# Optimization experiments

Hardware: AMD Instinct MI355X
Metric: run time of the kernel (lower is better)

The kernel has to match this reference:

```python
import jax, jax.numpy as jnp
import numpy as np

B, N, NPOINT, NSAMPLE = 4, 8192, 2048, 32
RADIUS = 0.5
IN_DIM, OUT_DIM, EXP = 64, 128, 4
GROUPS, EPS = 8, 1e-5


def fps(xyz, npoint):
    # xyz: [B,3,N] -> idx [B,npoint]. Deterministic start at index 0
    # (torch version uses a random start; math otherwise identical).
    b, _, n = xyz.shape
    binds = jnp.arange(b)

    def step(carry, _):
        dist_min, far = carry
        centroid = xyz[binds, :, far]                      # [B,3]
        d = jnp.sum((xyz - centroid[:, :, None]) ** 2, 1)  # [B,N]
        dist_min = jnp.minimum(dist_min, d)
        new_far = jnp.argmax(dist_min, axis=-1).astype(jnp.int32)
        return (dist_min, new_far), far

    init = (jnp.full((b, n), 1e10, dtype=xyz.dtype), jnp.zeros((b,), jnp.int32))
    _, idx = jax.lax.scan(step, init, None, length=npoint)
    return idx.T  # [B, npoint]


def gather(points, idx):
    # points: [B,C,N], idx: [B, ...] -> [B, C, ...]
    return jax.vmap(lambda p, i: p[:, i])(points, idx)


def ball_query(radius, nsample, xyz, new_xyz):
    # xyz: [B,3,N], new_xyz: [B,3,S] -> group_idx [B,S,nsample]
    n = xyz.shape[2]
    sq_s = jnp.sum(new_xyz ** 2, axis=1)  # [B,S]
    sq_n = jnp.sum(xyz ** 2, axis=1)      # [B,N]
    d = sq_s[:, :, None] + sq_n[:, None, :] - 2.0 * jnp.einsum('bcs,bcn->bsn', new_xyz, xyz)
    ar = jnp.arange(n, dtype=jnp.int32)
    idxv = jnp.where(d <= radius * radius, ar[None, None, :], n)  # out-of-ball -> N
    neg, _ = jax.lax.top_k(-idxv, nsample)  # nsample smallest indices
    gi = -neg                               # ascending, matches sort()[..., :nsample]
    first = gi[:, :, :1]
    first = jnp.where(first == n, 0, first)
    gi = jnp.where(gi == n, first, gi)
    return gi


def group_norm(x, gamma, beta):
    # x: [B,C,*spatial]; normalize per (group, all spatial)
    b, c = x.shape[0], x.shape[1]
    sp = x.shape[2:]
    xg = x.reshape(b, GROUPS, -1)
    mu = xg.mean(-1, keepdims=True)
    var = xg.var(-1, keepdims=True)
    xg = (xg - mu) * jax.lax.rsqrt(var + EPS)
    x = xg.reshape(b, c, *sp)
    gshape = (1, c) + (1,) * len(sp)
    return x * gamma.reshape(gshape) + beta.reshape(gshape)


def setup_inputs() -> dict:
    key = jax.random.key(0)
    ks = jax.random.split(key, 10)
    sc = lambda k, shape, s: jax.random.normal(k, shape, jnp.float32) * s
    ed = OUT_DIM * EXP
    return {
        'xyz': jax.random.normal(ks[0], (B, 3, N), jnp.float32),
        'points': jax.random.normal(ks[1], (B, IN_DIM, N), jnp.float32),
        't_emb': jax.random.normal(ks[2], (B, OUT_DIM), jnp.float32),
        'c_emb': jax.random.normal(ks[3], (B, OUT_DIM), jnp.float32),
        'w_mlp': sc(ks[4], (OUT_DIM, IN_DIM + 3), 0.1), 'b_mlp': jnp.zeros((OUT_DIM,), jnp.float32),
        'g0': jnp.ones((OUT_DIM,), jnp.float32), 'be0': jnp.zeros((OUT_DIM,), jnp.float32),
        'w1': sc(ks[5], (ed, OUT_DIM), 0.1), 'b1': jnp.zeros((ed,), jnp.float32),
        'g1': jnp.ones((ed,), jnp.float32), 'be1': jnp.zeros((ed,), jnp.float32),
        'w2': sc(ks[6], (OUT_DIM, ed), 0.1), 'b2': jnp.zeros((OUT_DIM,), jnp.float32),
        'g2': jnp.ones((OUT_DIM,), jnp.float32), 'be2': jnp.zeros((OUT_DIM,), jnp.float32),
        'wt': sc(ks[7], (2 * OUT_DIM, OUT_DIM), 0.02), 'bt': jnp.zeros((2 * OUT_DIM,), jnp.float32),
        'wc': sc(ks[8], (2 * OUT_DIM, OUT_DIM), 0.02), 'bc': jnp.zeros((2 * OUT_DIM,), jnp.float32),
    }


def reference(xyz, points, t_emb, c_emb, w_mlp, b_mlp, g0, be0, w1, b1, g1, be1, w2, b2, g2, be2, wt, bt, wc, bc):
    idx = fps(xyz, NPOINT)              # [B,S]
    new_xyz = gather(xyz, idx)          # [B,3,S]
    gi = ball_query(RADIUS, NSAMPLE, xyz, new_xyz)   # [B,S,ns]
    grouped_xyz = gather(xyz, gi)                    # [B,3,S,ns]
    gxn = grouped_xyz - new_xyz[:, :, :, None]
    gp = gather(points, gi)                          # [B,C,S,ns]
    feat = jnp.concatenate([gxn, gp], axis=1)        # [B,C+3,S,ns]
    x = jnp.einsum('oc,bcsk->bosk', w_mlp, feat) + b_mlp[None, :, None, None]
    x = jax.nn.silu(group_norm(x, g0, be0))
    x = x.max(axis=3)                                # [B,O,S]
    # InvResMLP with dual FiLM
    identity = x
    h = jnp.einsum('oc,bcs->bos', w1, x) + b1[None, :, None]
    h = jax.nn.silu(group_norm(h, g1, be1))
    h = jnp.einsum('oc,bcs->bos', w2, h) + b2[None, :, None]
    h = group_norm(h, g2, be2)
    st, sht = jnp.split(t_emb @ wt.T + bt, 2, axis=1)
    sc_, shc = jnp.split(c_emb @ wc.T + bc, 2, axis=1)
    scale = (st + sc_)[:, :, None]
    shift = (sht + shc)[:, :, None]
    new_points = h * (1.0 + scale) + shift + identity
    return (new_xyz, new_points)
```

## Files before the change

### kernel.cpp

```cpp
#include <hip/hip_runtime.h>
#include <math.h>

#define BB 4
#define NN 8192
#define SS 2048
#define KK 32
#define NGR 8

__global__ void k_sqn(const float* __restrict__ xyz, float* __restrict__ sqn) {
  int i = blockIdx.x * 256 + threadIdx.x;
  if (i >= BB * NN) return;
  int b = i >> 13, n = i & (NN - 1);
  const float* p = xyz + (size_t)b * 3 * NN;
  float x = p[n], y = p[NN + n], z = p[2 * NN + n];
  sqn[i] = __fadd_rn(__fadd_rn(__fmul_rn(x, x), __fmul_rn(y, y)), __fmul_rn(z, z));
}

__global__ void k_tr(const float* __restrict__ pts, float* __restrict__ ptst) {
  __shared__ float tile[64][65];
  int b = blockIdx.y;
  int n0 = blockIdx.x * 64;
  int t = threadIdx.x;
  {
    int n = t & 63, cq = t >> 6;
    for (int j = 0; j < 16; ++j) {
      int c = cq * 16 + j;
      tile[c][n] = pts[((size_t)b * 64 + c) * NN + n0 + n];
    }
  }
  __syncthreads();
  {
    int c = t & 63, nq = t >> 6;
    for (int j = 0; j < 16; ++j) {
      int nn2 = nq * 16 + j;
      ptst[((size_t)b * NN + n0 + nn2) * 64 + c] = tile[c][nn2];
    }
  }
}

__global__ void k_wt(const float* __restrict__ src, float* __restrict__ dst, int rows, int cols) {
  int i = blockIdx.x * 256 + threadIdx.x;
  if (i >= rows * cols) return;
  int r = i / cols, c = i - r * cols;
  dst[c * rows + r] = src[i];
}

__global__ void k_mod(const float* __restrict__ te, const float* __restrict__ ce,
                      const float* __restrict__ wt, const float* __restrict__ bt,
                      const float* __restrict__ wc, const float* __restrict__ bc,
                      float* __restrict__ scl, float* __restrict__ shf) {
  int t = blockIdx.x * 256 + threadIdx.x;
  if (t >= BB * 128) return;
  int b = t >> 7, o = t & 127;
  const float* tb = te + b * 128;
  const float* cb = ce + b * 128;
  float s1 = 0.f, s2 = 0.f, h1 = 0.f, h2 = 0.f;
  for (int c = 0; c < 128; ++c) {
    float tv = tb[c], cv = cb[c];
    s1 = fmaf(tv, wt[o * 128 + c], s1);
    h1 = fmaf(tv, wt[(o + 128) * 128 + c], h1);
    s2 = fmaf(cv, wc[o * 128 + c], s2);
    h2 = fmaf(cv, wc[(o + 128) * 128 + c], h2);
  }
  scl[t] = s1 + bt[o] + s2 + bc[o];
  shf[t] = h1 + bt[o + 128] + h2 + bc[o + 128];
}

template <int CTRL>
__device__ __forceinline__ unsigned long long kmax_dpp(unsigned long long key) {
  int lo = (int)(unsigned)(key & 0xffffffffull);
  int hi = (int)(unsigned)(key >> 32);
  int olo = __builtin_amdgcn_update_dpp(lo, lo, CTRL, 0xf, 0xf, false);
  int ohi = __builtin_amdgcn_update_dpp(hi, hi, CTRL, 0xf, 0xf, false);
  unsigned long long other =
      ((unsigned long long)(unsigned)ohi << 32) | (unsigned)olo;
  return other > key ? other : key;
}

#define FT 512
#define FPT (NN / FT)
#define FW (FT / 64)

__global__ __launch_bounds__(FT, 1) void k_fps(const float* __restrict__ xyz,
                                               float* __restrict__ newxyz) {
  int b = blockIdx.x;
  int t = threadIdx.x;
  const float* gx = xyz + (size_t)b * 3 * NN;
  const float* gy = gx + NN;
  const float* gz = gx + 2 * NN;
  __shared__ float4 p4[NN];
  __shared__ unsigned long long wk[2][FW];
  __shared__ int fars[SS];
  for (int i = t; i < NN; i += FT)
    p4[i] = make_float4(gx[i], gy[i], gz[i], 0.f);
  float px[FPT], py[FPT], pz[FPT], dm[FPT];
#pragma unroll
  for (int j = 0; j < FPT; ++j) {
    px[j] = gx[t + j * FT];
    py[j] = gy[t + j * FT];
    pz[j] = gz[t + j * FT];
    dm[j] = 1e10f;
    asm volatile("" : "+v"(px[j]), "+v"(py[j]), "+v"(pz[j]));
  }
  __syncthreads();
  int far = 0;
  for (int k = 0; k < SS; ++k) {
    float4 c = p4[far];
    if (t == 0) fars[k] = far;
    float bv = -1.f;
    int jb = 0;
#pragma unroll
    for (int j = 0; j < FPT; ++j) {
      float dx = __fsub_rn(px[j], c.x);
      float dy = __fsub_rn(py[j], c.y);
      float dz = __fsub_rn(pz[j], c.z);
      float d = __fadd_rn(__fadd_rn(__fmul_rn(dx, dx), __fmul_rn(dy, dy)), __fmul_rn(dz, dz));
      float m = fminf(dm[j], d);
      dm[j] = m;
      if (m > bv) { bv = m; jb = j; }
    }
    int bp = t + jb * FT;
    unsigned long long key =
        ((unsigned long long)__float_as_uint(bv) << 32) | (unsigned)(NN - 1 - bp);
    key = kmax_dpp<0xB1>(key);
    key = kmax_dpp<0x4E>(key);
    key = kmax_dpp<0x141>(key);
    key = kmax_dpp<0x140>(key);
    key = kmax_dpp<0x142>(key);
    key = kmax_dpp<0x143>(key);
    if ((t & 63) == 63) wk[k & 1][t >> 6] = key;
    __syncthreads();
    unsigned long long kg = wk[k & 1][t & (FW - 1)];
    kg = kmax_dpp<0xB1>(kg);
    kg = kmax_dpp<0x4E>(kg);
    kg = kmax_dpp<0x141>(kg);
    far = NN - 1 - (int)(unsigned)(kg & 0xffffffffull);
    far = __builtin_amdgcn_readfirstlane(far);
  }
  __syncthreads();
  float* ox = newxyz + (size_t)b * 3 * SS;
  for (int k = t; k < SS; k += FT) {
    float4 c = p4[fars[k]];
    ox[k] = c.x; ox[SS + k] = c.y; ox[2 * SS + k] = c.z;
  }
}

__global__ __launch_bounds__(256) void k_ballq(const float* __restrict__ xyz,
                                               const float* __restrict__ sqn,
                                               const float* __restrict__ newxyz,
                                               int* __restrict__ gi) {
  int wid = (blockIdx.x * 256 + threadIdx.x) >> 6;
  int lane = threadIdx.x & 63;
  if (wid >= BB * SS) return;
  int b = wid >> 11, s = wid & (SS - 1);
  const float* nx = newxyz + (size_t)b * 3 * SS;
  float sx = nx[s], sy = nx[SS + s], sz = nx[2 * SS + s];
  float ss = __fadd_rn(__fadd_rn(__fmul_rn(sx, sx), __fmul_rn(sy, sy)), __fmul_rn(sz, sz));
  const float* gx = xyz + (size_t)b * 3 * NN;
  const float* gy = gx + NN;
  const float* gz = gx + 2 * NN;
  const float* sn = sqn + (size_t)b * NN;
  int* go = gi + (size_t)wid * KK;
  int found = 0, first = 0;
  for (int n0 = 0; n0 < NN && found < KK; n0 += 64) {
    int n = n0 + lane;
    float x = gx[n], y = gy[n], z = gz[n];
    float ip = __fmul_rn(sx, x);
    ip = __fmaf_rn(sy, y, ip);
    ip = __fmaf_rn(sz, z, ip);
    float d = __fsub_rn(__fadd_rn(ss, sn[n]), __fmul_rn(2.0f, ip));
    bool pred = (d <= 0.25f);
    unsigned long long m = __ballot(pred);
    if (found == 0 && m) first = n0 + __ffsll((unsigned long long)m) - 1;
    if (pred) {
      int pos = found + __popcll(m & ((1ull << lane) - 1ull));
      if (pos < KK) go[pos] = n;
    }
    found += __popcll(m);
  }
  for (int p = found + lane; p < KK; p += 64) go[p] = first;
}

template <int PASS>
__global__ __launch_bounds__(256) void k_mlp0(
    const float* __restrict__ xyz, const float* __restrict__ ptst,
    const float* __restrict__ newxyz, const int* __restrict__ gi,
    const float* __restrict__ w0, const float* __restrict__ b0,
    double* __restrict__ dst, const float* __restrict__ fmu, const float* __restrict__ frs,
    const float* __restrict__ g0, const float* __restrict__ be0,
    float* __restrict__ xp) {
  __shared__ __align__(16) float w0L[128 * 67];
  __shared__ __align__(16) float featL[67 * 36];
  __shared__ int giL[KK];
  __shared__ float sS[NGR], sQ[NGR];
  __shared__ float maxL[128];
  int t = threadIdx.x;
  int bs = blockIdx.x;
  int b = bs >> 11;
  int s = bs & (SS - 1);
  for (int i = t; i < 128 * 67; i += 256) w0L[i] = w0[i];
  if (t < KK) giL[t] = gi[(size_t)bs * KK + t];
  if (PASS == 0 && t < NGR) { sS[t] = 0.f; sQ[t] = 0.f; }
  __syncthreads();
  {
    int k = t & 31, q = t >> 5;
    int idx = giL[k];
    const float4* src = (const float4*)(ptst + ((size_t)b * NN + idx) * 64 + q * 8);
    float4 v0 = src[0], v1 = src[1];
    int cb = 3 + q * 8;
    featL[(cb + 0) * 36 + k] = v0.x;
    featL[(cb + 1) * 36 + k] = v0.y;
    featL[(cb + 2) * 36 + k] = v0.z;
    featL[(cb + 3) * 36 + k] = v0.w;
    featL[(cb + 4) * 36 + k] = v1.x;
    featL[(cb + 5) * 36 + k] = v1.y;
    featL[(cb + 6) * 36 + k] = v1.z;
    featL[(cb + 7) * 36 + k] = v1.w;
    if (q == 0) {
      const float* gx = xyz + (size_t)b * 3 * NN;
      const float* nx = newxyz + (size_t)b * 3 * SS;
      featL[0 * 36 + k] = gx[idx] - nx[s];
      featL[1 * 36 + k] = gx[NN + idx] - nx[SS + s];
      featL[2 * 36 + k] = gx[2 * NN + idx] - nx[2 * SS + s];
    }
  }
  __syncthreads();
  int o = t & 127, kh = t >> 7;
  float acc[16];
#pragma unroll
  for (int j = 0; j < 16; ++j) acc[j] = 0.f;
  const float* wrow = w0L + o * 67;
  const float* fb = featL + kh * 16;
  for (int c = 0; c < 67; ++c) {
    float w = wrow[c];
    const float4* f4 = (const float4*)(fb + c * 36);
    float4 a = f4[0], b4 = f4[1], c4 = f4[2], d4 = f4[3];
    acc[0] = fmaf(w, a.x, acc[0]);    acc[1] = fmaf(w, a.y, acc[1]);
    acc[2] = fmaf(w, a.z, acc[2]);    acc[3] = fmaf(w, a.w, acc[3]);
    acc[4] = fmaf(w, b4.x, acc[4]);   acc[5] = fmaf(w, b4.y, acc[5]);
    acc[6] = fmaf(w, b4.z, acc[6]);   acc[7] = fmaf(w, b4.w, acc[7]);
    acc[8] = fmaf(w, c4.x, acc[8]);   acc[9] = fmaf(w, c4.y, acc[9]);
    acc[10] = fmaf(w, c4.z, acc[10]); acc[11] = fmaf(w, c4.w, acc[11]);
    acc[12] = fmaf(w, d4.x, acc[12]); acc[13] = fmaf(w, d4.y, acc[13]);
    acc[14] = fmaf(w, d4.z, acc[14]); acc[15] = fmaf(w, d4.w, acc[15]);
  }
  float bb = b0[o];
  int g = o >> 4;
  if (PASS == 0) {
    float ps = 0.f, pq = 0.f;
#pragma unroll
    for (int j = 0; j < 16; ++j) { float v = acc[j] + bb; ps += v; pq += v * v; }
    atomicAdd(&sS[g], ps);
    atomicAdd(&sQ[g], pq);
    __syncthreads();
    if (t < NGR) {
      atomicAdd(&dst[b * NGR + t], (double)sS[t]);
      atomicAdd(&dst[32 + b * NGR + t], (double)sQ[t]);
    }
  } else {
    float mu = fmu[b * NGR + g], rs = frs[b * NGR + g];
    float ga = g0[o], be = be0[o];
    float m = -3.4e38f;
#pragma unroll
    for (int j = 0; j < 16; ++j) {
      float v = acc[j] + bb;
      v = (v - mu) * rs * ga + be;
      v = v / (1.f + expf(-v));
      m = fmaxf(m, v);
    }
    if (kh == 0) maxL[o] = m;
    __syncthreads();
    if (kh == 1) xp[(size_t)bs * 128 + o] = fmaxf(maxL[o], m);
  }
}

__global__ void k_fin(const double* __restrict__ dst, float* __restrict__ fmu,
                      float* __restrict__ frs, double cntInv) {
  int i = threadIdx.x;
  if (i >= BB * NGR) return;
  double m = dst[i] * cntInv;
  double q = dst[32 + i] * cntInv;
  double var = q - m * m;
  fmu[i] = (float)m;
  frs[i] = (float)rsqrt(var + 1e-5);
}

__global__ __launch_bounds__(256) void k_mlp1(
    const float* __restrict__ xp, const float* __restrict__ w1t,
    const float* __restrict__ b1, float* __restrict__ h1, double* __restrict__ dst) {
  __shared__ __align__(16) float xpL[8 * 128];
  __shared__ float sS[NGR], sQ[NGR];
  int t = threadIdx.x;
  int bs0 = blockIdx.x * 8;
  int b = bs0 >> 11;
  if (t < NGR) { sS[t] = 0.f; sQ[t] = 0.f; }
  {
    int idx4 = t >> 5, l = t & 31;
    ((float4*)xpL)[idx4 * 32 + l] = ((const float4*)(xp + (size_t)bs0 * 128))[idx4 * 32 + l];
  }
  __syncthreads();
  float acc0[8], acc1[8];
#pragma unroll
  for (int i = 0; i < 8; ++i) { acc0[i] = 0.f; acc1[i] = 0.f; }
  for (int c4 = 0; c4 < 32; ++c4) {
    float wa0 = w1t[(c4 * 4 + 0) * 512 + t];
    float wa1 = w1t[(c4 * 4 + 1) * 512 + t];
    float wa2 = w1t[(c4 * 4 + 2) * 512 + t];
    float wa3 = w1t[(c4 * 4 + 3) * 512 + t];
    float wb0 = w1t[(c4 * 4 + 0) * 512 + 256 + t];
    float wb1 = w1t[(c4 * 4 + 1) * 512 + 256 + t];
    float wb2 = w1t[(c4 * 4 + 2) * 512 + 256 + t];
    float wb3 = w1t[(c4 * 4 + 3) * 512 + 256 + t];
#pragma unroll
    for (int si = 0; si < 8; ++si) {
      float4 xv = *(const float4*)(xpL + si * 128 + c4 * 4);
      acc0[si] = fmaf(wa0, xv.x, acc0[si]);
      acc0[si] = fmaf(wa1, xv.y, acc0[si]);
      acc0[si] = fmaf(wa2, xv.z, acc0[si]);
      acc0[si] = fmaf(wa3, xv.w, acc0[si]);
      acc1[si] = fmaf(wb0, xv.x, acc1[si]);
      acc1[si] = fmaf(wb1, xv.y, acc1[si]);
      acc1[si] = fmaf(wb2, xv.z, acc1[si]);
      acc1[si] = fmaf(wb3, xv.w, acc1[si]);
    }
  }
  float ba = b1[t], bbv = b1[256 + t];
  float ps0 = 0.f, pq0 = 0.f, ps1 = 0.f, pq1 = 0.f;
#pragma unroll
  for (int si = 0; si < 8; ++si) {
    float va = acc0[si] + ba;
    float vb = acc1[si] + bbv;
    h1[(size_t)(bs0 + si) * 512 + t] = va;
    h1[(size_t)(bs0 + si) * 512 + 256 + t] = vb;
    ps0 += va; pq0 += va * va;
    ps1 += vb; pq1 += vb * vb;
  }
  atomicAdd(&sS[t >> 6], ps0);
  atomicAdd(&sQ[t >> 6], pq0);
  atomicAdd(&sS[4 + (t >> 6)], ps1);
  atomicAdd(&sQ[4 + (t >> 6)], pq1);
  __syncthreads();
  if (t < NGR) {
    atomicAdd(&dst[b * NGR + t], (double)sS[t]);
    atomicAdd(&dst[32 + b * NGR + t], (double)sQ[t]);
  }
}

__global__ __launch_bounds__(256) void k_mlp2(
    const float* __restrict__ h1, const float* __restrict__ w2t,
    const float* __restrict__ b2, const float* __restrict__ fmu1, const float* __restrict__ frs1,
    const float* __restrict__ g1, const float* __restrict__ be1,
    float* __restrict__ h2, double* __restrict__ dst) {
  __shared__ __align__(16) float hL[8 * 512];
  __shared__ float sS[NGR], sQ[NGR];
  int t = threadIdx.x;
  int bs0 = blockIdx.x * 8;
  int b = bs0 >> 11;
  if (t < NGR) { sS[t] = 0.f; sQ[t] = 0.f; }
  {
    int si = t >> 5, l = t & 31;
    int c0 = l * 16;
    int g = c0 >> 6;
    float mu = fmu1[b * NGR + g], rs = frs1[b * NGR + g];
    const float* src = h1 + (size_t)(bs0 + si) * 512 + c0;
#pragma unroll
    for (int j = 0; j < 16; ++j) {
      float v = src[j];
      v = (v - mu) * rs * g1[c0 + j] + be1[c0 + j];
      v = v / (1.f + expf(-v));
      hL[si * 512 + c0 + j] = v;
    }
  }
  __syncthreads();
  int o = t & 127, sh = t >> 7;
  float acc[4] = {0.f, 0.f, 0.f, 0.f};
  for (int c4 = 0; c4 < 128; ++c4) {
    float w0v = w2t[(c4 * 4 + 0) * 128 + o];
    float w1v = w2t[(c4 * 4 + 1) * 128 + o];
    float w2v = w2t[(c4 * 4 + 2) * 128 + o];
    float w3v = w2t[(c4 * 4 + 3) * 128 + o];
#pragma unroll
    for (int m = 0; m < 4; ++m) {
      float4 hq = *(const float4*)(hL + (sh * 4 + m) * 512 + c4 * 4);
      acc[m] = fmaf(w0v, hq.x, acc[m]);
      acc[m] = fmaf(w1v, hq.y, acc[m]);
      acc[m] = fmaf(w2v, hq.z, acc[m]);
      acc[m] = fmaf(w3v, hq.w, acc[m]);
    }
  }
  float bb = b2[o];
  float ps = 0.f, pq = 0.f;
#pragma unroll
  for (int m = 0; m < 4; ++m) {
    float v = acc[m] + bb;
    h2[(size_t)(bs0 + sh * 4 + m) * 128 + o] = v;
    ps += v; pq += v * v;
  }
  atomicAdd(&sS[o >> 4], ps);
  atomicAdd(&sQ[o >> 4], pq);
  __syncthreads();
  if (t < NGR) {
    atomicAdd(&dst[b * NGR + t], (double)sS[t]);
    atomicAdd(&dst[32 + b * NGR + t], (double)sQ[t]);
  }
}

__global__ void k_final(const float* __restrict__ h2, const float* __restrict__ xp,
                        const float* __restrict__ fmu2, const float* __restrict__ frs2,
                        const float* __restrict__ g2, const float* __restrict__ be2,
                        const float* __restrict__ scl, const float* __restrict__ shf,
                        float* __restrict__ out) {
  int f = blockIdx.x * 256 + threadIdx.x;
  if (f >= BB * 128 * SS) return;
  int s = f & (SS - 1);
  int o = (f >> 11) & 127;
  int b = f >> 18;
  int g = o >> 4;
  float v = h2[((size_t)b * SS + s) * 128 + o];
  v = (v - fmu2[b * NGR + g]) * frs2[b * NGR + g] * g2[o] + be2[o];
  float idv = xp[((size_t)b * SS + s) * 128 + o];
  out[f] = v * (1.f + scl[b * 128 + o]) + shf[b * 128 + o] + idv;
}

extern "C" void kernel_launch(void* const* d_in, const int* in_sizes, int n_in,
                              void* d_out, int out_size, void* d_ws, size_t ws_size,
                              hipStream_t stream) {
  const float* xyz = (const float*)d_in[0];
  const float* pts = (const float*)d_in[1];
  const float* te = (const float*)d_in[2];
  const float* ce = (const float*)d_in[3];
  const float* w0 = (const float*)d_in[4];
  const float* b0 = (const float*)d_in[5];
  const float* g0 = (const float*)d_in[6];
  const float* be0 = (const float*)d_in[7];
  const float* w1 = (const float*)d_in[8];
  const float* b1 = (const float*)d_in[9];
  const float* g1 = (const float*)d_in[10];
  const float* be1 = (const float*)d_in[11];
  const float* w2 = (const float*)d_in[12];
  const float* b2 = (const float*)d_in[13];
  const float* g2 = (const float*)d_in[14];
  const float* be2 = (const float*)d_in[15];
  const float* wt = (const float*)d_in[16];
  const float* bt = (const float*)d_in[17];
  const float* wc = (const float*)d_in[18];
  const float* bc = (const float*)d_in[19];

  char* ws = (char*)d_ws;
  size_t off = 0;
  auto alloc = [&](size_t bytes) {
    void* p = ws + off;
    off += (bytes + 255) & ~(size_t)255;
    return p;
  };
  float* ptst = (float*)alloc((size_t)BB * NN * 64 * 4);
  float* sqn = (float*)alloc((size_t)BB * NN * 4);
  int* gi = (int*)alloc((size_t)BB * SS * KK * 4);
  float* xp = (float*)alloc((size_t)BB * SS * 128 * 4);
  float* h1 = (float*)alloc((size_t)BB * SS * 512 * 4);
  float* h2 = (float*)alloc((size_t)BB * SS * 128 * 4);
  float* w1t = (float*)alloc(512 * 128 * 4);
  float* w2t = (float*)alloc(512 * 128 * 4);
  float* scl = (float*)alloc(BB * 128 * 4);
  float* shf = (float*)alloc(BB * 128 * 4);
  double* dstat = (double*)alloc(3 * 64 * 8);
  float* fmu = (float*)alloc(3 * 32 * 4);
  float* frs = (float*)alloc(3 * 32 * 4);

  float* newxyz = (float*)d_out;
  float* outnp = (float*)d_out + (size_t)BB * 3 * SS;

  hipMemsetAsync(dstat, 0, 3 * 64 * 8, stream);
  k_sqn<<<BB * NN / 256, 256, 0, stream>>>(xyz, sqn);
  k_tr<<<dim3(NN / 64, BB), 256, 0, stream>>>(pts, ptst);
  k_wt<<<(512 * 128 + 255) / 256, 256, 0, stream>>>(w1, w1t, 512, 128);
  k_wt<<<(512 * 128 + 255) / 256, 256, 0, stream>>>(w2, w2t, 128, 512);
  k_mod<<<2, 256, 0, stream>>>(te, ce, wt, bt, wc, bc, scl, shf);
  k_fps<<<BB, FT, 0, stream>>>(xyz, newxyz);
  k_ballq<<<BB * SS / 4, 256, 0, stream>>>(xyz, sqn, newxyz, gi);
  k_mlp0<0><<<BB * SS, 256, 0, stream>>>(xyz, ptst, newxyz, gi, w0, b0, dstat, fmu, frs, g0, be0, xp);
  k_fin<<<1, 64, 0, stream>>>(dstat, fmu, frs, 1.0 / (16.0 * SS * KK));
  k_mlp0<1><<<BB * SS, 256, 0, stream>>>(xyz, ptst, newxyz, gi, w0, b0, dstat, fmu, frs, g0, be0, xp);
  k_mlp1<<<BB * SS / 8, 256, 0, stream>>>(xp, w1t, b1, h1, dstat + 64);
  k_fin<<<1, 64, 0, stream>>>(dstat + 64, fmu + 32, frs + 32, 1.0 / (64.0 * SS));
  k_mlp2<<<BB * SS / 8, 256, 0, stream>>>(h1, w2t, b2, fmu + 32, frs + 32, g1, be1, h2, dstat + 128);
  k_fin<<<1, 64, 0, stream>>>(dstat + 128, fmu + 64, frs + 64, 1.0 / (16.0 * SS));
  k_final<<<BB * 128 * SS / 256, 256, 0, stream>>>(h2, xp, fmu + 64, frs + 64, g2, be2, scl, shf, outnp);
}
```

Before: 2.329 ms.

## Fuse prologue kernels into FPS launch and split argmax into max-then-min-index reductions

New measurement: 2.221 ms. 1.05x faster.

```diff
diff --git a/kernel.cpp b/kernel.cpp
--- a/kernel.cpp
+++ b/kernel.cpp
@@ -7,141 +7,175 @@
 #define KK 32
 #define NGR 8
 
-__global__ void k_sqn(const float* __restrict__ xyz, float* __restrict__ sqn) {
-  int i = blockIdx.x * 256 + threadIdx.x;
-  if (i >= BB * NN) return;
-  int b = i >> 13, n = i & (NN - 1);
-  const float* p = xyz + (size_t)b * 3 * NN;
-  float x = p[n], y = p[NN + n], z = p[2 * NN + n];
-  sqn[i] = __fadd_rn(__fadd_rn(__fmul_rn(x, x), __fmul_rn(y, y)), __fmul_rn(z, z));
-}
-
-__global__ void k_tr(const float* __restrict__ pts, float* __restrict__ ptst) {
-  __shared__ float tile[64][65];
-  int b = blockIdx.y;
-  int n0 = blockIdx.x * 64;
-  int t = threadIdx.x;
-  {
-    int n = t & 63, cq = t >> 6;
-    for (int j = 0; j < 16; ++j) {
-      int c = cq * 16 + j;
-      tile[c][n] = pts[((size_t)b * 64 + c) * NN + n0 + n];
-    }
-  }
-  __syncthreads();
-  {
-    int c = t & 63, nq = t >> 6;
-    for (int j = 0; j < 16; ++j) {
-      int nn2 = nq * 16 + j;
-      ptst[((size_t)b * NN + n0 + nn2) * 64 + c] = tile[c][nn2];
-    }
-  }
-}
-
-__global__ void k_wt(const float* __restrict__ src, float* __restrict__ dst, int rows, int cols) {
-  int i = blockIdx.x * 256 + threadIdx.x;
-  if (i >= rows * cols) return;
-  int r = i / cols, c = i - r * cols;
-  dst[c * rows + r] = src[i];
-}
-
-__global__ void k_mod(const float* __restrict__ te, const float* __restrict__ ce,
-                      const float* __restrict__ wt, const float* __restrict__ bt,
-                      const float* __restrict__ wc, const float* __restrict__ bc,
-                      float* __restrict__ scl, float* __restrict__ shf) {
-  int t = blockIdx.x * 256 + threadIdx.x;
-  if (t >= BB * 128) return;
-  int b = t >> 7, o = t & 127;
-  const float* tb = te + b * 128;
-  const float* cb = ce + b * 128;
-  float s1 = 0.f, s2 = 0.f, h1 = 0.f, h2 = 0.f;
-  for (int c = 0; c < 128; ++c) {
-    float tv = tb[c], cv = cb[c];
-    s1 = fmaf(tv, wt[o * 128 + c], s1);
-    h1 = fmaf(tv, wt[(o + 128) * 128 + c], h1);
-    s2 = fmaf(cv, wc[o * 128 + c], s2);
-    h2 = fmaf(cv, wc[(o + 128) * 128 + c], h2);
-  }
-  scl[t] = s1 + bt[o] + s2 + bc[o];
-  shf[t] = h1 + bt[o + 128] + h2 + bc[o + 128];
-}
-
 template <int CTRL>
-__device__ __forceinline__ unsigned long long kmax_dpp(unsigned long long key) {
-  int lo = (int)(unsigned)(key & 0xffffffffull);
-  int hi = (int)(unsigned)(key >> 32);
-  int olo = __builtin_amdgcn_update_dpp(lo, lo, CTRL, 0xf, 0xf, false);
-  int ohi = __builtin_amdgcn_update_dpp(hi, hi, CTRL, 0xf, 0xf, false);
-  unsigned long long other =
-      ((unsigned long long)(unsigned)ohi << 32) | (unsigned)olo;
-  return other > key ? other : key;
-}
-
-#define FT 512
+__device__ __forceinline__ unsigned umaxdpp(unsigned v) {
+  int o = __builtin_amdgcn_update_dpp((int)v, (int)v, CTRL, 0xf, 0xf, false);
+  unsigned u = (unsigned)o;
+  return u > v ? u : v;
+}
+template <int CTRL>
+__device__ __forceinline__ int imindpp(int v) {
+  int o = __builtin_amdgcn_update_dpp(v, v, CTRL, 0xf, 0xf, false);
+  return o < v ? o : v;
+}
+
+#define FT 256
 #define FPT (NN / FT)
 #define FW (FT / 64)
 
-__global__ __launch_bounds__(FT, 1) void k_fps(const float* __restrict__ xyz,
-                                               float* __restrict__ newxyz) {
-  int b = blockIdx.x;
+#define NB_SQN (BB * NN / 256)
+#define NB_TR ((NN / 64) * BB)
+#define NB_WT 32
+#define NB_MOD 2
+#define NB_TOTAL (BB + NB_SQN + NB_TR + NB_WT + NB_MOD)
+
+__global__ __launch_bounds__(FT, 1) void k_fps(
+    const float* __restrict__ xyz, float* __restrict__ newxyz,
+    float* __restrict__ sqn, const float* __restrict__ pts, float* __restrict__ ptst,
+    const float* __restrict__ w1, float* __restrict__ w1t,
+    const float* __restrict__ w2, float* __restrict__ w2t,
+    const float* __restrict__ te, const float* __restrict__ ce,
+    const float* __restrict__ wt, const float* __restrict__ bt,
+    const float* __restrict__ wc, const float* __restrict__ bc,
+    float* __restrict__ scl, float* __restrict__ shf) {
+  __shared__ float4 p4[NN];
+  __shared__ int fars[SS];
+  __shared__ unsigned wkd[2][FW];
+  __shared__ int wki[2][FW];
   int t = threadIdx.x;
-  const float* gx = xyz + (size_t)b * 3 * NN;
-  const float* gy = gx + NN;
-  const float* gz = gx + 2 * NN;
-  __shared__ float4 p4[NN];
-  __shared__ unsigned long long wk[2][FW];
-  __shared__ int fars[SS];
-  for (int i = t; i < NN; i += FT)
-    p4[i] = make_float4(gx[i], gy[i], gz[i], 0.f);
-  float px[FPT], py[FPT], pz[FPT], dm[FPT];
-#pragma unroll
-  for (int j = 0; j < FPT; ++j) {
-    px[j] = gx[t + j * FT];
-    py[j] = gy[t + j * FT];
-    pz[j] = gz[t + j * FT];
-    dm[j] = 1e10f;
-    asm volatile("" : "+v"(px[j]), "+v"(py[j]), "+v"(pz[j]));
-  }
-  __syncthreads();
-  int far = 0;
-  for (int k = 0; k < SS; ++k) {
-    float4 c = p4[far];
-    if (t == 0) fars[k] = far;
-    float bv = -1.f;
-    int jb = 0;
+  int bid = blockIdx.x;
+
+  if (bid < BB) {
+    int b = bid;
+    const float* gx = xyz + (size_t)b * 3 * NN;
+    const float* gy = gx + NN;
+    const float* gz = gx + 2 * NN;
+    for (int i = t; i < NN; i += FT)
+      p4[i] = make_float4(gx[i], gy[i], gz[i], 0.f);
+    float px[FPT], py[FPT], pz[FPT], dm[FPT];
 #pragma unroll
     for (int j = 0; j < FPT; ++j) {
-      float dx = __fsub_rn(px[j], c.x);
-      float dy = __fsub_rn(py[j], c.y);
-      float dz = __fsub_rn(pz[j], c.z);
-      float d = __fadd_rn(__fadd_rn(__fmul_rn(dx, dx), __fmul_rn(dy, dy)), __fmul_rn(dz, dz));
-      float m = fminf(dm[j], d);
-      dm[j] = m;
-      if (m > bv) { bv = m; jb = j; }
-    }
-    int bp = t + jb * FT;
-    unsigned long long key =
-        ((unsigned long long)__float_as_uint(bv) << 32) | (unsigned)(NN - 1 - bp);
-    key = kmax_dpp<0xB1>(key);
-    key = kmax_dpp<0x4E>(key);
-    key = kmax_dpp<0x141>(key);
-    key = kmax_dpp<0x140>(key);
-    key = kmax_dpp<0x142>(key);
-    key = kmax_dpp<0x143>(key);
-    if ((t & 63) == 63) wk[k & 1][t >> 6] = key;
+      px[j] = gx[t + j * FT];
+      py[j] = gy[t + j * FT];
+      pz[j] = gz[t + j * FT];
+      dm[j] = 1e10f;
+      asm volatile("" : "+v"(px[j]), "+v"(py[j]), "+v"(pz[j]));
+    }
     __syncthreads();
-    unsigned long long kg = wk[k & 1][t & (FW - 1)];
-    kg = kmax_dpp<0xB1>(kg);
-    kg = kmax_dpp<0x4E>(kg);
-    kg = kmax_dpp<0x141>(kg);
-    far = NN - 1 - (int)(unsigned)(kg & 0xffffffffull);
-    far = __builtin_amdgcn_readfirstlane(far);
-  }
-  __syncthreads();
-  float* ox = newxyz + (size_t)b * 3 * SS;
-  for (int k = t; k < SS; k += FT) {
-    float4 c = p4[fars[k]];
-    ox[k] = c.x; ox[SS + k] = c.y; ox[2 * SS + k] = c.z;
+    int far = 0;
+    for (int k = 0; k < SS; ++k) {
+      float4 c = p4[far];
+      if (t == 0) fars[k] = far;
+      float bv = -1.f;
+      int jb = 0;
+#pragma unroll
+      for (int j = 0; j < FPT; ++j) {
+        float dx = __fsub_rn(px[j], c.x);
+        float dy = __fsub_rn(py[j], c.y);
+        float dz = __fsub_rn(pz[j], c.z);
+        float d = __fadd_rn(__fadd_rn(__fmul_rn(dx, dx), __fmul_rn(dy, dy)), __fmul_rn(dz, dz));
+        float m = fminf(dm[j], d);
+        dm[j] = m;
+        if (m > bv) { bv = m; jb = j; }
+      }
+      int bp = t + jb * FT;
+      unsigned bvb = __float_as_uint(bv);
+      unsigned kv = bvb;
+      kv = umaxdpp<0xB1>(kv);
+      kv = umaxdpp<0x4E>(kv);
+      kv = umaxdpp<0x141>(kv);
+      kv = umaxdpp<0x140>(kv);
+      kv = umaxdpp<0x142>(kv);
+      kv = umaxdpp<0x143>(kv);
+      unsigned wmb = (unsigned)__builtin_amdgcn_readlane((int)kv, 63);
+      int cand = (bvb == wmb) ? bp : 0x7fffffff;
+      cand = imindpp<0xB1>(cand);
+      cand = imindpp<0x4E>(cand);
+      cand = imindpp<0x141>(cand);
+      cand = imindpp<0x140>(cand);
+      cand = imindpp<0x142>(cand);
+      cand = imindpp<0x143>(cand);
+      if ((t & 63) == 63) { wkd[k & 1][t >> 6] = wmb; wki[k & 1][t >> 6] = cand; }
+      __syncthreads();
+      unsigned md = wkd[k & 1][t & (FW - 1)];
+      int mi = wki[k & 1][t & (FW - 1)];
+      unsigned bm = md;
+      bm = umaxdpp<0xB1>(bm);
+      bm = umaxdpp<0x4E>(bm);
+      int c2 = (md == bm) ? mi : 0x7fffffff;
+      c2 = imindpp<0xB1>(c2);
+      c2 = imindpp<0x4E>(c2);
+      far = __builtin_amdgcn_readfirstlane(c2);
+    }
+    __syncthreads();
+    float* ox = newxyz + (size_t)b * 3 * SS;
+    for (int k = t; k < SS; k += FT) {
+      float4 c = p4[fars[k]];
+      ox[k] = c.x; ox[SS + k] = c.y; ox[2 * SS + k] = c.z;
+    }
+    return;
+  }
+  bid -= BB;
+
+  if (bid < NB_SQN) {
+    int i = bid * 256 + t;
+    int b = i >> 13, n = i & (NN - 1);
+    const float* p = xyz + (size_t)b * 3 * NN;
+    float x = p[n], y = p[NN + n], z = p[2 * NN + n];
+    sqn[i] = __fadd_rn(__fadd_rn(__fmul_rn(x, x), __fmul_rn(y, y)), __fmul_rn(z, z));
+    return;
+  }
+  bid -= NB_SQN;
+
+  if (bid < NB_TR) {
+    float* tile = (float*)p4;
+    int b = bid >> 7;
+    int n0 = (bid & 127) << 6;
+    {
+      int n = t & 63, cq = t >> 6;
+      for (int j = 0; j < 16; ++j) {
+        int c = cq * 16 + j;
+        tile[c * 65 + n] = pts[((size_t)b * 64 + c) * NN + n0 + n];
+      }
+    }
+    __syncthreads();
+    {
+      int c = t & 63, nq = t >> 6;
+      for (int j = 0; j < 16; ++j) {
+        int nn2 = nq * 16 + j;
+        ptst[((size_t)b * NN + n0 + nn2) * 64 + c] = tile[c * 65 + nn2];
+      }
+    }
+    return;
+  }
+  bid -= NB_TR;
+
+  if (bid < NB_WT) {
+    for (int i = bid * 256 + t; i < 512 * 128; i += NB_WT * 256) {
+      int r = i >> 7, c = i & 127;
+      w1t[c * 512 + r] = w1[i];
+      int r2 = i >> 9, c2 = i & 511;
+      w2t[c2 * 128 + r2] = w2[i];
+    }
+    return;
+  }
+  bid -= NB_WT;
+
+  {
+    int tg = bid * 256 + t;
+    int b = tg >> 7, o = tg & 127;
+    const float* tb = te + b * 128;
+    const float* cb = ce + b * 128;
+    float s1 = 0.f, s2 = 0.f, h1 = 0.f, h2 = 0.f;
+    for (int c = 0; c < 128; ++c) {
+      float tv = tb[c], cv = cb[c];
+      s1 = fmaf(tv, wt[o * 128 + c], s1);
+      h1 = fmaf(tv, wt[(o + 128) * 128 + c], h1);
+      s2 = fmaf(cv, wc[o * 128 + c], s2);
+      h2 = fmaf(cv, wc[(o + 128) * 128 + c], h2);
+    }
+    scl[tg] = s1 + bt[o] + s2 + bc[o];
+    shf[tg] = h1 + bt[o + 128] + h2 + bc[o + 128];
   }
 }
 
@@ -471,12 +505,8 @@
   float* outnp = (float*)d_out + (size_t)BB * 3 * SS;
 
   hipMemsetAsync(dstat, 0, 3 * 64 * 8, stream);
-  k_sqn<<<BB * NN / 256, 256, 0, stream>>>(xyz, sqn);
-  k_tr<<<dim3(NN / 64, BB), 256, 0, stream>>>(pts, ptst);
-  k_wt<<<(512 * 128 + 255) / 256, 256, 0, stream>>>(w1, w1t, 512, 128);
-  k_wt<<<(512 * 128 + 255) / 256, 256, 0, stream>>>(w2, w2t, 128, 512);
-  k_mod<<<2, 256, 0, stream>>>(te, ce, wt, bt, wc, bc, scl, shf);
-  k_fps<<<BB, FT, 0, stream>>>(xyz, newxyz);
+  k_fps<<<NB_TOTAL, FT, 0, stream>>>(xyz, newxyz, sqn, pts, ptst, w1, w1t, w2, w2t,
+                                     te, ce, wt, bt, wc, bc, scl, shf);
   k_ballq<<<BB * SS / 4, 256, 0, stream>>>(xyz, sqn, newxyz, gi);
   k_mlp0<0><<<BB * SS, 256, 0, stream>>>(xyz, ptst, newxyz, gi, w0, b0, dstat, fmu, frs, g0, be0, xp);
   k_fin<<<1, 64, 0, stream>>>(dstat, fmu, frs, 1.0 / (16.0 * SS * KK));
```
